# Kernel optimization log

Measured on AMD Instinct MI355X. Metric: run time of the kernel, lower is better.

Reference implementation:

```python
import jax, jax.numpy as jnp
import numpy as np

D, NH, HD = 256, 8, 32          # d_model, heads, head_dim
NPTS, NLAY, FF = 4, 6, 1024     # dec_n_points, decoder layers, ffn dim
BS, HS, WS = 4, 96, 96
N = HS * WS                     # flattened source tokens (single level)
NQ = 300                        # object queries
EPS = 1e-5


def setup_inputs() -> dict:
    key = jax.random.key(0)
    ks = iter(jax.random.split(key, 48))

    def nrm(shape, s=0.05):
        return (jax.random.normal(next(ks), shape) * s).astype(jnp.float32)

    inp = {
        "aps": jax.random.normal(next(ks), (BS, N, D), jnp.float32),
        "dvs": jax.random.normal(next(ks), (BS, N, D), jnp.float32),
        "query_embeds": jax.random.normal(next(ks), (NQ, 2 * D), jnp.float32),
        "valid_ratios": jnp.ones((BS, 2), jnp.float32),
        # fusion gating linears (stored as (in, out); y = x @ W + b)
        "aps_w1": nrm((D, D)), "aps_b1": jnp.zeros((D,), jnp.float32),
        "aps_w2": nrm((D, D)), "aps_b2": jnp.zeros((D,), jnp.float32),
        "dvs_w1": nrm((D, D)), "dvs_b1": jnp.zeros((D,), jnp.float32),
        "dvs_w2": nrm((D, D)), "dvs_b2": jnp.zeros((D,), jnp.float32),
        "ref_w": nrm((D, 2)), "ref_b": jnp.zeros((2,), jnp.float32),
        # per-decoder-layer params, stacked along leading NLAY axis
        "sa_qkv_w": nrm((NLAY, D, 3 * D)), "sa_qkv_b": jnp.zeros((NLAY, 3 * D), jnp.float32),
        "sa_out_w": nrm((NLAY, D, D)), "sa_out_b": jnp.zeros((NLAY, D), jnp.float32),
        "off_w": nrm((NLAY, D, NH * NPTS * 2), 0.01),
        "off_b": nrm((NLAY, NH * NPTS * 2), 2.0),
        "attn_w": nrm((NLAY, D, NH * NPTS)), "attn_b": jnp.zeros((NLAY, NH * NPTS), jnp.float32),
        "val_w": nrm((NLAY, D, D)), "val_b": jnp.zeros((NLAY, D), jnp.float32),
        "cout_w": nrm((NLAY, D, D)), "cout_b": jnp.zeros((NLAY, D), jnp.float32),
        "ln1_w": jnp.ones((NLAY, D), jnp.float32), "ln1_b": jnp.zeros((NLAY, D), jnp.float32),
        "ln2_w": jnp.ones((NLAY, D), jnp.float32), "ln2_b": jnp.zeros((NLAY, D), jnp.float32),
        "ln3_w": jnp.ones((NLAY, D), jnp.float32), "ln3_b": jnp.zeros((NLAY, D), jnp.float32),
        "ffn_w1": nrm((NLAY, D, FF)), "ffn_b1": jnp.zeros((NLAY, FF), jnp.float32),
        "ffn_w2": nrm((NLAY, FF, D)), "ffn_b2": jnp.zeros((NLAY, D), jnp.float32),
        "mask": jnp.zeros((BS, N), bool),
        "spatial_shapes": jnp.array([[HS, WS]], jnp.int32),
    }
    return inp


def _layer_norm(x, w, b):
    mu = jnp.mean(x, -1, keepdims=True)
    var = jnp.mean((x - mu) ** 2, -1, keepdims=True)
    return (x - mu) * jax.lax.rsqrt(var + EPS) * w + b


def _forward(aps, dvs, query_embeds, valid_ratios,
             aps_w1, aps_b1, aps_w2, aps_b2,
             dvs_w1, dvs_b1, dvs_w2, dvs_b2,
             ref_w, ref_b,
             sa_qkv_w, sa_qkv_b, sa_out_w, sa_out_b,
             off_w, off_b, attn_w, attn_b, val_w, val_b, cout_w, cout_b,
             ln1_w, ln1_b, ln2_w, ln2_b, ln3_w, ln3_b,
             ffn_w1, ffn_b1, ffn_w2, ffn_b2,
             mask, spatial_shapes):
    bs = aps.shape[0]
    inv_sqrt_d = np.float32(1.0 / np.sqrt(D))
    # ---- cross-modal gating. Original computes full (N,N) QK^T then sums the
    # last axis; sum_j q_i.k_j == q_i . (sum_j k_j), so we use the O(N*d) form.
    aps_gate = jnp.einsum('bnd,bd->bn', aps @ aps_w1 + aps_b1,
                          jnp.sum(aps @ aps_w2 + aps_b2, axis=1)) * inv_sqrt_d
    dvs_gate = jnp.einsum('bnd,bd->bn', dvs @ dvs_w1 + dvs_b1,
                          jnp.sum(dvs @ dvs_w2 + dvs_b2, axis=1)) * inv_sqrt_d
    gate = jax.nn.softmax(jnp.stack([aps_gate, dvs_gate], -1), -1)  # (bs,N,2)
    src = gate[..., :1] * aps + gate[..., 1:] * dvs

    qpos = jnp.broadcast_to(query_embeds[None, :, :D], (bs, NQ, D))
    out = jnp.broadcast_to(query_embeds[None, :, D:], (bs, NQ, D))
    ref_pts = jax.nn.sigmoid(qpos @ ref_w + ref_b)                 # (bs,NQ,2)

    Hs = spatial_shapes[0, 0]
    Ws = spatial_shapes[0, 1]
    # reference_points[:, :, None] * valid_ratios[:, None][:, None] -> (bs,NQ,1,2)
    rp_in = ref_pts[:, :, None, :] * valid_ratios[:, None, None, :]
    inv_sqrt_hd = np.float32(1.0 / np.sqrt(HD))

    for l in range(NLAY):
        # ---- self attention (q=k=tgt+query_pos, v=tgt)
        qk = out + qpos
        qh = (qk @ sa_qkv_w[l, :, :D] + sa_qkv_b[l, :D]).reshape(bs, NQ, NH, HD)
        kh = (qk @ sa_qkv_w[l, :, D:2 * D] + sa_qkv_b[l, D:2 * D]).reshape(bs, NQ, NH, HD)
        vh = (out @ sa_qkv_w[l, :, 2 * D:] + sa_qkv_b[l, 2 * D:]).reshape(bs, NQ, NH, HD)
        att = jax.nn.softmax(jnp.einsum('bqhd,bkhd->bhqk', qh, kh) * inv_sqrt_hd, -1)
        sa = jnp.einsum('bhqk,bkhd->bqhd', att, vh).reshape(bs, NQ, D) @ sa_out_w[l] + sa_out_b[l]
        out = _layer_norm(out + sa, ln2_w[l], ln2_b[l])

        # ---- MSDeformAttn cross attention (single level)
        q = out + qpos
        value = jnp.where(mask[:, :, None], 0.0, src @ val_w[l] + val_b[l])
        value = value.reshape(bs, -1, NH, HD).transpose(0, 2, 1, 3)   # (bs,NH,N,HD)
        offs = (q @ off_w[l] + off_b[l]).reshape(bs, NQ, NH, 1, NPTS, 2)
        aw = jax.nn.softmax((q @ attn_w[l] + attn_b[l]).reshape(bs, NQ, NH, NPTS), -1)
        normalizer = jnp.stack([Ws, Hs]).astype(q.dtype)              # [W, H]
        loc = (rp_in[:, :, None, :, None, :] + offs / normalizer)[:, :, :, 0]  # (bs,NQ,NH,NPTS,2)
        # bilinear sampling == grid_sample(align_corners=False, padding=zeros)
        x = loc[..., 0] * Ws - 0.5
        y = loc[..., 1] * Hs - 0.5
        x0 = jnp.floor(x); y0 = jnp.floor(y)
        wx1 = x - x0; wy1 = y - y0

        def corner(xi, yi, w):
            valid = (xi >= 0) & (xi <= Ws - 1) & (yi >= 0) & (yi <= Hs - 1)
            idx = (jnp.clip(yi, 0, Hs - 1) * Ws + jnp.clip(xi, 0, Ws - 1)).astype(jnp.int32)
            idx = idx.transpose(0, 2, 1, 3).reshape(bs, NH, NQ * NPTS, 1)
            v = jnp.take_along_axis(value, idx, axis=2)              # (bs,NH,NQ*NPTS,HD)
            v = v.reshape(bs, NH, NQ, NPTS, HD).transpose(0, 2, 1, 3, 4)
            return v * (w * valid)[..., None]

        samp = (corner(x0, y0, (1 - wx1) * (1 - wy1))
                + corner(x0 + 1, y0, wx1 * (1 - wy1))
                + corner(x0, y0 + 1, (1 - wx1) * wy1)
                + corner(x0 + 1, y0 + 1, wx1 * wy1))                 # (bs,NQ,NH,NPTS,HD)
        ca = jnp.einsum('bqhp,bqhpd->bqhd', aw, samp).reshape(bs, NQ, D) @ cout_w[l] + cout_b[l]
        out = _layer_norm(out + ca, ln1_w[l], ln1_b[l])

        # ---- FFN
        ff = jax.nn.relu(out @ ffn_w1[l] + ffn_b1[l]) @ ffn_w2[l] + ffn_b2[l]
        out = _layer_norm(out + ff, ln3_w[l], ln3_b[l])

    # return_intermediate_dec=False -> decoder returns (output, reference_points)
    return out, ref_pts, ref_pts


def reference(aps, dvs, query_embeds, valid_ratios,
              aps_w1, aps_b1, aps_w2, aps_b2,
              dvs_w1, dvs_b1, dvs_w2, dvs_b2,
              ref_w, ref_b,
              sa_qkv_w, sa_qkv_b, sa_out_w, sa_out_b,
              off_w, off_b, attn_w, attn_b, val_w, val_b, cout_w, cout_b,
              ln1_w, ln1_b, ln2_w, ln2_b, ln3_w, ln3_b,
              ffn_w1, ffn_b1, ffn_w2, ffn_b2,
              mask, spatial_shapes):
    return _forward(aps, dvs, query_embeds, valid_ratios,
                    aps_w1, aps_b1, aps_w2, aps_b2,
                    dvs_w1, dvs_b1, dvs_w2, dvs_b2,
                    ref_w, ref_b,
                    sa_qkv_w, sa_qkv_b, sa_out_w, sa_out_b,
                    off_w, off_b, attn_w, attn_b, val_w, val_b, cout_w, cout_b,
                    ln1_w, ln1_b, ln2_w, ln2_b, ln3_w, ln3_b,
                    ffn_w1, ffn_b1, ffn_w2, ffn_b2,
                    mask, spatial_shapes)
```

## Files before the change

kernel.cpp:

```cpp
#include <hip/hip_runtime.h>
#include <math.h>

#define D 256
#define NHD 8
#define HDIM 32
#define NPTS 4
#define NLAY 6
#define FFD 1024
#define BSZ 4
#define NSRC 9216
#define NQ 300
#define NROWS (BSZ*NQ)
#define NVROWS (BSZ*NSRC)
#define CCHK 256
#define VSTRIDE 1536
#define LNEPS 1e-5f

typedef __attribute__((ext_vector_type(8))) short short8v;
typedef __attribute__((ext_vector_type(4))) float f32x4;

#define GLOAD_LDS(g, l) __builtin_amdgcn_global_load_lds( \
    (const __attribute__((address_space(1))) void*)(g), \
    (__attribute__((address_space(3))) void*)(l), 16, 0, 0)

__device__ __forceinline__ unsigned short f2bf(float f){
  unsigned u = __float_as_uint(f);
  unsigned r = (u + 0x7FFFu + ((u>>16)&1u)) >> 16;
  return (unsigned short)r;
}
__device__ __forceinline__ float bf2f(unsigned short u){
  return __uint_as_float(((unsigned)u)<<16);
}

__device__ __forceinline__ float wred_sum(float v){
#pragma unroll
  for(int o=32;o>=1;o>>=1) v += __shfl_xor(v,o,64);
  return v;
}
__device__ __forceinline__ float bred_sum(float v, float* s){
  v = wred_sum(v);
  int lane = threadIdx.x & 63, wid = threadIdx.x >> 6;
  if(lane==0) s[wid]=v;
  __syncthreads();
  float r = s[0]+s[1]+s[2]+s[3];
  __syncthreads();
  return r;
}

__global__ void colsum_partial(const float* __restrict__ aps, const float* __restrict__ dvs,
                               float* __restrict__ pA, float* __restrict__ pD){
  __shared__ float4 sA[4][64]; __shared__ float4 sD[4][64];
  int blk = blockIdx.x; int b = blk / CCHK; int c = blk % CCHK;
  int t = threadIdx.x; int cl = t & 63; int rg = t >> 6;
  const int rows = NSRC / CCHK;
  size_t base = ((size_t)b*NSRC + (size_t)c*rows)*D + cl*4;
  float4 sa = make_float4(0.f,0.f,0.f,0.f), sd = sa;
  for(int r=rg; r<rows; r+=4){
    float4 va = *(const float4*)(aps + base + (size_t)r*D);
    float4 vd = *(const float4*)(dvs + base + (size_t)r*D);
    sa.x+=va.x; sa.y+=va.y; sa.z+=va.z; sa.w+=va.w;
    sd.x+=vd.x; sd.y+=vd.y; sd.z+=vd.z; sd.w+=vd.w;
  }
  sA[rg][cl]=sa; sD[rg][cl]=sd;
  __syncthreads();
  if(t < 64){
    float4 r0=sA[0][t],r1=sA[1][t],r2=sA[2][t],r3=sA[3][t];
    float4 o; o.x=r0.x+r1.x+r2.x+r3.x; o.y=r0.y+r1.y+r2.y+r3.y;
    o.z=r0.z+r1.z+r2.z+r3.z; o.w=r0.w+r1.w+r2.w+r3.w;
    *(float4*)(pA + ((size_t)b*CCHK+c)*D + t*4) = o;
  } else if(t < 128){
    int u=t-64;
    float4 r0=sD[0][u],r1=sD[1][u],r2=sD[2][u],r3=sD[3][u];
    float4 o; o.x=r0.x+r1.x+r2.x+r3.x; o.y=r0.y+r1.y+r2.y+r3.y;
    o.z=r0.z+r1.z+r2.z+r3.z; o.w=r0.w+r1.w+r2.w+r3.w;
    *(float4*)(pD + ((size_t)b*CCHK+c)*D + u*4) = o;
  }
}

__global__ void gate_s2(const float* __restrict__ pA, const float* __restrict__ pD,
                        const float* __restrict__ w2a, const float* __restrict__ b2a,
                        const float* __restrict__ w2d, const float* __restrict__ b2d,
                        const float* __restrict__ b1a, const float* __restrict__ b1d,
                        float* __restrict__ s2, float* __restrict__ cAB){
  __shared__ float sums[D]; __shared__ float red[4];
  int blk = blockIdx.x; int b = blk>>1; int mod = blk&1;
  int t = threadIdx.x;
  const float* pX = mod? pD : pA;
  const float* w2 = mod? w2d : w2a;
  const float* b2 = mod? b2d : b2a;
  const float* b1 = mod? b1d : b1a;
  float s=0.f;
  for(int c=0;c<CCHK;++c) s += pX[((size_t)b*CCHK+c)*D+t];
  sums[t]=s; __syncthreads();
  float v=0.f;
  for(int i=0;i<D;++i) v += sums[i]*w2[(size_t)i*D+t];
  v += (float)NSRC * b2[t];
  s2[(size_t)blk*D + t] = v;
  float c = bred_sum(b1[t]*v, red);
  if(t==0) cAB[mod*BSZ + b] = c;
}

__global__ void gate_t(const float* __restrict__ w1a, const float* __restrict__ w1d,
                       const float* __restrict__ s2,
                       float* __restrict__ tA, float* __restrict__ tD){
  int gw = blockIdx.x*4 + (threadIdx.x>>6);
  int lane = threadIdx.x & 63;
  int i = gw & 255; int bm = gw >> 8;
  int mod = bm & 1, b = bm >> 1;
  const float* w1 = mod? w1d : w1a;
  const float* s2v = s2 + (size_t)bm*D;
  float4 wv = *(const float4*)(w1 + (size_t)i*D + lane*4);
  float4 sv = *(const float4*)(s2v + lane*4);
  float d = wv.x*sv.x + wv.y*sv.y + wv.z*sv.z + wv.w*sv.w;
  d = wred_sum(d);
  if(lane==0){
    if(mod) tD[b*D+i] = d; else tA[b*D+i] = d;
  }
}

__global__ void gate_src(const float* __restrict__ aps, const float* __restrict__ dvs,
                         const float* __restrict__ tA, const float* __restrict__ tD,
                         const float* __restrict__ cAB, unsigned short* __restrict__ srcb){
  int w = threadIdx.x >> 6, lane = threadIdx.x & 63;
  size_t row = (size_t)blockIdx.x*4 + w;
  int b = (int)(row / NSRC);
  const float4* ap = (const float4*)(aps + row*D);
  const float4* dp = (const float4*)(dvs + row*D);
  const float4* tap = (const float4*)(tA + (size_t)b*D);
  const float4* tdp = (const float4*)(tD + (size_t)b*D);
  float4 a = ap[lane], dd = dp[lane], ta = tap[lane], td = tdp[lane];
  float ga = a.x*ta.x + a.y*ta.y + a.z*ta.z + a.w*ta.w;
  float gd = dd.x*td.x + dd.y*td.y + dd.z*td.z + dd.w*td.w;
  ga = (wred_sum(ga) + cAB[b]) * 0.0625f;
  gd = (wred_sum(gd) + cAB[BSZ+b]) * 0.0625f;
  float m = fmaxf(ga,gd);
  float ea = expf(ga-m), ed = expf(gd-m);
  float inv = 1.f/(ea+ed);
  float wa = ea*inv, wd = ed*inv;
  ushort4 o;
  o.x = f2bf(wa*a.x + wd*dd.x); o.y = f2bf(wa*a.y + wd*dd.y);
  o.z = f2bf(wa*a.z + wd*dd.z); o.w = f2bf(wa*a.w + wd*dd.w);
  ((ushort4*)(srcb + row*D))[lane] = o;
}

__global__ void wconv_all(const float* __restrict__ valw, const float* __restrict__ saqkvw,
                          const float* __restrict__ saoutw, const float* __restrict__ coutw,
                          const float* __restrict__ ffw1, const float* __restrict__ ffw2,
                          unsigned short* __restrict__ valT, unsigned short* __restrict__ qkvT,
                          unsigned short* __restrict__ saoutT, unsigned short* __restrict__ coutT,
                          unsigned short* __restrict__ ff1T, unsigned short* __restrict__ ff2T){
  __shared__ float tile[32][33];
  int bid = blockIdx.x;
  const float* W; unsigned short* Bt; int K, N, rel;
  if(bid < 384)      { W=valw;   Bt=valT;   K=256;  N=256;  rel=bid; }
  else if(bid < 1536){ W=saqkvw; Bt=qkvT;   K=256;  N=768;  rel=bid-384; }
  else if(bid < 1920){ W=saoutw; Bt=saoutT; K=256;  N=256;  rel=bid-1536; }
  else if(bid < 2304){ W=coutw;  Bt=coutT;  K=256;  N=256;  rel=bid-1920; }
  else if(bid < 3840){ W=ffw1;   Bt=ff1T;   K=256;  N=1024; rel=bid-2304; }
  else               { W=ffw2;   Bt=ff2T;   K=1024; N=256;  rel=bid-3840; }
  int nk = K>>5, nn = N>>5, tpl = nk*nn;
  int l = rel/tpl, rem = rel%tpl;
  int tk = rem % nk, tn = rem / nk;
  int tx = threadIdx.x & 31, ty = threadIdx.x >> 5;
  const float* Wl = W + (size_t)l*K*N;
  unsigned short* Btl = Bt + (size_t)l*N*K;
#pragma unroll
  for(int i=0;i<4;++i)
    tile[ty+i*8][tx] = Wl[(size_t)(tk*32+ty+i*8)*N + tn*32+tx];
  __syncthreads();
#pragma unroll
  for(int i=0;i<4;++i)
    Btl[(size_t)(tn*32+ty+i*8)*K + tk*32+tx] = f2bf(tile[tx][ty+i*8]);
}

__global__ void init_out_ref(const float* __restrict__ qe, const float* __restrict__ refw,
                             const float* __restrict__ refb,
                             float* __restrict__ outb, unsigned short* __restrict__ out_bf,
                             unsigned short* __restrict__ outpos_bf,
                             float* __restrict__ refp, float* __restrict__ dout){
  __shared__ float red[4];
  int q = blockIdx.x, t = threadIdx.x;
  float pos = qe[(size_t)q*2*D + t];
  float tgt = qe[(size_t)q*2*D + D + t];
  unsigned short tb = f2bf(tgt), tpb = f2bf(tgt+pos);
  for(int b=0;b<BSZ;++b){
    outb[((size_t)b*NQ+q)*D + t] = tgt;
    out_bf[((size_t)b*NQ+q)*D + t] = tb;
    outpos_bf[((size_t)b*NQ+q)*D + t] = tpb;
  }
  float d0 = bred_sum(pos*refw[t*2+0], red);
  float d1 = bred_sum(pos*refw[t*2+1], red);
  if(t<2){
    float dot = (t==0? d0 : d1) + refb[t];
    float r = 1.f/(1.f+expf(-dot));
    refp[q*2+t] = r;
    const size_t o1 = (size_t)BSZ*NQ*D;
    const size_t o2 = o1 + (size_t)BSZ*NQ*2;
    for(int b=0;b<BSZ;++b){
      dout[o1 + (b*NQ+q)*2 + t] = r;
      dout[o2 + (b*NQ+q)*2 + t] = r;
    }
  }
}

__global__ __launch_bounds__(256, 4) void gemmb(
    const unsigned short* __restrict__ A,
    const unsigned short* __restrict__ A2,
    int ncut,
    const unsigned short* __restrict__ Bt,
    const float* __restrict__ bias,
    float* __restrict__ Cf, unsigned short* __restrict__ Cb,
    int M, int K, int N, int relu){
  __shared__ unsigned short As[64][40];
  __shared__ unsigned short Bs[64][40];
  int n0 = blockIdx.x*64, m0 = blockIdx.y*64;
  const unsigned short* Asrc = (A2 && n0 >= ncut) ? A2 : A;
  int t = threadIdx.x, wave = t>>6, lane = t&63;
  int wm = (wave>>1)*32, wn = (wave&1)*32;
  int hi = lane>>4, lo = lane&15;
  int sr = t>>2, sc = (t&3)*8;
  f32x4 acc[2][2];
#pragma unroll
  for(int i=0;i<2;++i)
#pragma unroll
    for(int j=0;j<2;++j)
#pragma unroll
      for(int r=0;r<4;++r) acc[i][j][r]=0.f;
  for(int k0=0;k0<K;k0+=32){
    uint4 av = make_uint4(0,0,0,0);
    int arow = m0+sr;
    if(arow < M) av = *(const uint4*)(Asrc + (size_t)arow*K + k0 + sc);
    *(uint4*)&As[sr][sc] = av;
    *(uint4*)&Bs[sr][sc] = *(const uint4*)(Bt + (size_t)(n0+sr)*K + k0 + sc);
    __syncthreads();
    short8v a0 = *(short8v*)&As[wm+lo][hi*8];
    short8v a1 = *(short8v*)&As[wm+16+lo][hi*8];
    short8v b0 = *(short8v*)&Bs[wn+lo][hi*8];
    short8v b1 = *(short8v*)&Bs[wn+16+lo][hi*8];
    acc[0][0] = __builtin_amdgcn_mfma_f32_16x16x32_bf16(a0,b0,acc[0][0],0,0,0);
    acc[0][1] = __builtin_amdgcn_mfma_f32_16x16x32_bf16(a0,b1,acc[0][1],0,0,0);
    acc[1][0] = __builtin_amdgcn_mfma_f32_16x16x32_bf16(a1,b0,acc[1][0],0,0,0);
    acc[1][1] = __builtin_amdgcn_mfma_f32_16x16x32_bf16(a1,b1,acc[1][1],0,0,0);
    __syncthreads();
  }
#pragma unroll
  for(int mf=0;mf<2;++mf){
#pragma unroll
    for(int nf=0;nf<2;++nf){
      int col = n0 + wn + nf*16 + lo;
      float bv = bias[col];
#pragma unroll
      for(int r=0;r<4;++r){
        int row = m0 + wm + mf*16 + hi*4 + r;
        if(row < M){
          float v = acc[mf][nf][r] + bv;
          if(relu) v = fmaxf(v, 0.f);
          if(Cf) Cf[(size_t)row*N+col] = v;
          if(Cb) Cb[(size_t)row*N+col] = f2bf(v);
        }
      }
    }
  }
}

__global__ __launch_bounds__(256, 4) void mfma_value6(
    const unsigned short* __restrict__ Abf,
    const unsigned short* __restrict__ Bt,
    const float* __restrict__ bias,
    const unsigned char* __restrict__ rowmask,
    unsigned short* __restrict__ C){
  __shared__ unsigned short As[128][32];
  __shared__ unsigned short Bs[128][32];
  int id = blockIdx.x;
  int swz = (id & 7)*432 + (id >> 3);
  int m0 = (swz/12)*128, n0 = (swz%12)*128;
  int t = threadIdx.x;
  int wave = t>>6, lane = t&63;
  int wm = (wave>>1)*64, wn = (wave&1)*64;
  f32x4 acc[4][4];
#pragma unroll
  for(int i=0;i<4;++i)
#pragma unroll
    for(int j=0;j<4;++j)
#pragma unroll
      for(int r=0;r<4;++r) acc[i][j][r]=0.f;

  int colx = ((lane&3) ^ ((lane>>3)&3)) * 8;
  const unsigned short* Ag = Abf + (size_t)(m0 + wave*32 + (lane>>2))*256 + colx;
  const unsigned short* Bg = Bt  + (size_t)(n0 + wave*32 + (lane>>2))*256 + colx;
  unsigned short* Al0 = &As[wave*32][0];
  unsigned short* Al1 = &As[wave*32+16][0];
  unsigned short* Bl0 = &Bs[wave*32][0];
  unsigned short* Bl1 = &Bs[wave*32+16][0];

  int hi = lane>>4, lo = lane&15;
  int sx = (hi ^ ((lo>>1)&3)) * 8;

  for(int k0=0;k0<256;k0+=32){
    GLOAD_LDS(Ag + k0,           Al0);
    GLOAD_LDS(Ag + k0 + 16*256,  Al1);
    GLOAD_LDS(Bg + k0,           Bl0);
    GLOAD_LDS(Bg + k0 + 16*256,  Bl1);
    __syncthreads();
    short8v a[4], bb[4];
#pragma unroll
    for(int mf=0;mf<4;++mf) a[mf]  = *(short8v*)&As[wm+mf*16+lo][sx];
#pragma unroll
    for(int nf=0;nf<4;++nf) bb[nf] = *(short8v*)&Bs[wn+nf*16+lo][sx];
#pragma unroll
    for(int mf=0;mf<4;++mf)
#pragma unroll
      for(int nf=0;nf<4;++nf)
        acc[mf][nf] = __builtin_amdgcn_mfma_f32_16x16x32_bf16(a[mf], bb[nf], acc[mf][nf], 0,0,0);
    __syncthreads();
  }
#pragma unroll
  for(int mf=0;mf<4;++mf){
    int rbase = m0 + wm + mf*16 + (lane>>4)*4;
#pragma unroll
    for(int nf=0;nf<4;++nf){
      int col = n0 + wn + nf*16 + (lane&15);
      float bv = bias[col];
#pragma unroll
      for(int r=0;r<4;++r){
        int row = rbase + r;
        float v = acc[mf][nf][r] + bv;
        if(rowmask[row]) v = 0.f;
        C[(size_t)row*VSTRIDE + col] = f2bf(v);
      }
    }
  }
}

__global__ __launch_bounds__(256) void self_attn_mfma(
    const unsigned short* __restrict__ qkvh,
    unsigned short* __restrict__ sa){
  __shared__ unsigned short P[64][328];
  __shared__ unsigned short Vt[32][328];
  int blk = blockIdx.x;
  int qt = blk % 5; int bh = blk / 5; int h = bh % NHD; int b = bh / NHD;
  int t = threadIdx.x, wv = t>>6, lane = t&63;
  int hi = lane>>4, lo = lane&15;
  {
    int c = t & 31, rb = t >> 5;
    for(int r = rb; r < 320; r += 8){
      unsigned short v = 0;
      if(r < 300) v = qkvh[(size_t)(b*300+r)*768 + 512 + h*32 + c];
      Vt[c][r] = v;
    }
  }
  __syncthreads();
  int m0 = qt*64 + wv*16;
  int qr = m0 + lo; if(qr > 299) qr = 299;
  short8v aq = *(const short8v*)(qkvh + (size_t)(b*300+qr)*768 + h*32 + hi*8);
  f32x4 s[19];
#pragma unroll
  for(int nt=0; nt<19; ++nt){
    int kr = nt*16 + lo; if(kr > 299) kr = 299;
    short8v bk = *(const short8v*)(qkvh + (size_t)(b*300+kr)*768 + 256 + h*32 + hi*8);
    f32x4 z; z[0]=0.f; z[1]=0.f; z[2]=0.f; z[3]=0.f;
    s[nt] = __builtin_amdgcn_mfma_f32_16x16x32_bf16(aq, bk, z, 0,0,0);
  }
  const float kSc = 0.25506009837f;
  float inv[4];
#pragma unroll
  for(int ri=0; ri<4; ++ri){
    float m = -1e30f;
#pragma unroll
    for(int nt=0; nt<19; ++nt){
      if(nt*16+lo < 300) m = fmaxf(m, s[nt][ri]);
    }
#pragma unroll
    for(int o=8;o>=1;o>>=1) m = fmaxf(m, __shfl_xor(m,o,64));
    float sum = 0.f;
#pragma unroll
    for(int nt=0; nt<19; ++nt){
      float p = 0.f;
      if(nt*16+lo < 300) p = exp2f((s[nt][ri]-m)*kSc);
      sum += p;
      P[wv*16 + hi*4 + ri][nt*16 + lo] = f2bf(p);
    }
    P[wv*16 + hi*4 + ri][304 + lo] = 0;
#pragma unroll
    for(int o=8;o>=1;o>>=1) sum += __shfl_xor(sum,o,64);
    inv[ri] = 1.f/sum;
  }
  f32x4 o0, o1;
#pragma unroll
  for(int r=0;r<4;++r){ o0[r]=0.f; o1[r]=0.f; }
#pragma unroll
  for(int kt=0; kt<10; ++kt){
    short8v ap = *(short8v*)&P[wv*16 + lo][kt*32 + hi*8];
    short8v b0 = *(short8v*)&Vt[lo][kt*32 + hi*8];
    short8v b1 = *(short8v*)&Vt[16+lo][kt*32 + hi*8];
    o0 = __builtin_amdgcn_mfma_f32_16x16x32_bf16(ap, b0, o0, 0,0,0);
    o1 = __builtin_amdgcn_mfma_f32_16x16x32_bf16(ap, b1, o1, 0,0,0);
  }
#pragma unroll
  for(int ri=0; ri<4; ++ri){
    int r = m0 + hi*4 + ri;
    if(r < 300){
      size_t base = (size_t)(b*300+r)*256 + h*32;
      sa[base + lo]      = f2bf(o0[ri]*inv[ri]);
      sa[base + 16 + lo] = f2bf(o1[ri]*inv[ri]);
    }
  }
}

__global__ void residual_ln(const float* __restrict__ base, const float* __restrict__ delta,
                            const float* __restrict__ lw, const float* __restrict__ lb,
                            float* __restrict__ dstf, unsigned short* __restrict__ dstb,
                            unsigned short* __restrict__ dstp, const float* __restrict__ qe){
  int w = threadIdx.x >> 6, lane = threadIdx.x & 63;
  size_t row = (size_t)blockIdx.x*4 + w;
  float4 bv = ((const float4*)(base + row*D))[lane];
  float4 dv = ((const float4*)(delta + row*D))[lane];
  float4 v; v.x=bv.x+dv.x; v.y=bv.y+dv.y; v.z=bv.z+dv.z; v.w=bv.w+dv.w;
  float s = wred_sum(v.x+v.y+v.z+v.w);
  float mean = s * (1.f/D);
  float4 c; c.x=v.x-mean; c.y=v.y-mean; c.z=v.z-mean; c.w=v.w-mean;
  float vs = wred_sum(c.x*c.x + c.y*c.y + c.z*c.z + c.w*c.w);
  float inv = rsqrtf(vs*(1.f/D) + LNEPS);
  float4 wv = ((const float4*)lw)[lane];
  float4 lbv = ((const float4*)lb)[lane];
  float4 y; y.x=c.x*inv*wv.x+lbv.x; y.y=c.y*inv*wv.y+lbv.y;
  y.z=c.z*inv*wv.z+lbv.z; y.w=c.w*inv*wv.w+lbv.w;
  ((float4*)(dstf + row*D))[lane] = y;
  if(dstb){
    ushort4 o; o.x=f2bf(y.x); o.y=f2bf(y.y); o.z=f2bf(y.z); o.w=f2bf(y.w);
    ((ushort4*)(dstb + row*D))[lane] = o;
  }
  if(dstp){
    int q = (int)(row % NQ);
    float4 qv = ((const float4*)(qe + (size_t)q*2*D))[lane];
    ushort4 o; o.x=f2bf(y.x+qv.x); o.y=f2bf(y.y+qv.y);
    o.z=f2bf(y.z+qv.z); o.w=f2bf(y.w+qv.w);
    ((ushort4*)(dstp + row*D))[lane] = o;
  }
}

__global__ void deform_attn_ln(const float* __restrict__ base, const float* __restrict__ delta,
                               const float* __restrict__ lnw, const float* __restrict__ lnb,
                               float* __restrict__ outb,
                               const float* __restrict__ qe,
                               const float* __restrict__ offw, const float* __restrict__ offb,
                               const float* __restrict__ attnw, const float* __restrict__ attnb,
                               const unsigned short* __restrict__ value, const float* __restrict__ refp,
                               const float* __restrict__ vr, const int* __restrict__ sshape,
                               unsigned short* __restrict__ ca){
  __shared__ float qrow[D];
  __shared__ float part[96][2];
  __shared__ float proj[96];
  __shared__ float red[4];
  int row = blockIdx.x; int b = row / NQ; int q = row % NQ;
  int t = threadIdx.x;
  float v = base[(size_t)row*D+t] + delta[(size_t)row*D+t];
  float mean = bred_sum(v, red) * (1.f/D);
  float c = v - mean;
  float var = bred_sum(c*c, red) * (1.f/D);
  float y = c * rsqrtf(var + LNEPS) * lnw[t] + lnb[t];
  outb[(size_t)row*D+t] = y;
  qrow[t] = y + qe[(size_t)q*2*D + t];
  __syncthreads();
  if(t < 192){
    int col = t >> 1, half = t & 1;
    float acc = 0.f;
    if(col < 64){
      const float* W = offw;
      for(int k=half*128; k<half*128+128; ++k) acc += qrow[k]*W[(size_t)k*64 + col];
    } else {
      const float* W = attnw; int cc = col-64;
      for(int k=half*128; k<half*128+128; ++k) acc += qrow[k]*W[(size_t)k*32 + cc];
    }
    part[col][half] = acc;
  }
  __syncthreads();
  if(t < 96) proj[t] = part[t][0] + part[t][1] + (t<64 ? offb[t] : attnb[t-64]);
  __syncthreads();

  int h = t>>5, hd = t&31;
  float Hf = (float)sshape[0], Wf = (float)sshape[1];
  int Ws = sshape[1];
  float rx = refp[q*2+0] * vr[b*2+0];
  float ry = refp[q*2+1] * vr[b*2+1];
  const float* lg = &proj[64 + h*4];
  float m = fmaxf(fmaxf(lg[0],lg[1]),fmaxf(lg[2],lg[3]));
  float e[4]; float esum=0.f;
#pragma unroll
  for(int p=0;p<4;++p){ e[p]=expf(lg[p]-m); esum+=e[p]; }
  float einv = 1.f/esum;
  const float* ofr = &proj[h*8];
  const unsigned short* vbase = value + ((size_t)b*NSRC)*VSTRIDE + h*HDIM + hd;
  float acc = 0.f;
#pragma unroll
  for(int p=0;p<NPTS;++p){
    float lx = rx + ofr[p*2+0]/Wf;
    float ly = ry + ofr[p*2+1]/Hf;
    float x = lx*Wf - 0.5f, y2 = ly*Hf - 0.5f;
    float x0 = floorf(x), y0 = floorf(y2);
    float wx = x-x0, wy = y2-y0;
    float sample = 0.f;
#pragma unroll
    for(int cy=0;cy<2;++cy){
#pragma unroll
      for(int cx=0;cx<2;++cx){
        float xi = x0+cx, yi = y0+cy;
        float wgt = (cx? wx : 1.f-wx) * (cy? wy : 1.f-wy);
        bool valid = (xi>=0.f)&&(xi<=Wf-1.f)&&(yi>=0.f)&&(yi<=Hf-1.f);
        if(valid){
          int idx = (int)fminf(fmaxf(yi,0.f),Hf-1.f)*Ws + (int)fminf(fmaxf(xi,0.f),Wf-1.f);
          sample += wgt * bf2f(vbase[(size_t)idx*VSTRIDE]);
        }
      }
    }
    acc += (e[p]*einv) * sample;
  }
  ca[(size_t)row*D + h*HDIM + hd] = f2bf(acc);
}

extern "C" void kernel_launch(void* const* d_in, const int* in_sizes, int n_in,
                              void* d_out, int out_size, void* d_ws, size_t ws_size,
                              hipStream_t stream){
  const float* aps=(const float*)d_in[0];
  const float* dvs=(const float*)d_in[1];
  const float* qe =(const float*)d_in[2];
  const float* vr =(const float*)d_in[3];
  const float* aps_w1=(const float*)d_in[4]; const float* aps_b1=(const float*)d_in[5];
  const float* aps_w2=(const float*)d_in[6]; const float* aps_b2=(const float*)d_in[7];
  const float* dvs_w1=(const float*)d_in[8]; const float* dvs_b1=(const float*)d_in[9];
  const float* dvs_w2=(const float*)d_in[10]; const float* dvs_b2=(const float*)d_in[11];
  const float* ref_w=(const float*)d_in[12]; const float* ref_b=(const float*)d_in[13];
  const float* saqkvw=(const float*)d_in[14]; const float* saqkvb=(const float*)d_in[15];
  const float* saoutw=(const float*)d_in[16]; const float* saoutb=(const float*)d_in[17];
  const float* offw=(const float*)d_in[18]; const float* offb=(const float*)d_in[19];
  const float* attnw=(const float*)d_in[20]; const float* attnb=(const float*)d_in[21];
  const float* valw=(const float*)d_in[22]; const float* valb=(const float*)d_in[23];
  const float* coutw=(const float*)d_in[24]; const float* coutb=(const float*)d_in[25];
  const float* ln1w=(const float*)d_in[26]; const float* ln1b=(const float*)d_in[27];
  const float* ln2w=(const float*)d_in[28]; const float* ln2b=(const float*)d_in[29];
  const float* ln3w=(const float*)d_in[30]; const float* ln3b=(const float*)d_in[31];
  const float* ffw1=(const float*)d_in[32]; const float* ffb1=(const float*)d_in[33];
  const float* ffw2=(const float*)d_in[34]; const float* ffb2=(const float*)d_in[35];
  const unsigned char* mask=(const unsigned char*)d_in[36];
  const int* sshape=(const int*)d_in[37];
  float* out = (float*)d_out;

  char* wsb = (char*)d_ws;
  size_t o = 0;
  unsigned short* srcb   = (unsigned short*)(wsb+o); o += (size_t)NVROWS*D*2;
  unsigned short* valT   = (unsigned short*)(wsb+o); o += (size_t)NLAY*D*D*2;
  unsigned short* qkvT   = (unsigned short*)(wsb+o); o += (size_t)NLAY*3*D*D*2;
  unsigned short* saoutT = (unsigned short*)(wsb+o); o += (size_t)NLAY*D*D*2;
  unsigned short* coutT  = (unsigned short*)(wsb+o); o += (size_t)NLAY*D*D*2;
  unsigned short* ff1T   = (unsigned short*)(wsb+o); o += (size_t)NLAY*D*FFD*2;
  unsigned short* ff2T   = (unsigned short*)(wsb+o); o += (size_t)NLAY*FFD*D*2;
  unsigned short* value  = (unsigned short*)(wsb+o); o += (size_t)NVROWS*VSTRIDE*2;
  float* pA    = (float*)(wsb+o); o += (size_t)BSZ*CCHK*D*4;
  float* pD    = (float*)(wsb+o); o += (size_t)BSZ*CCHK*D*4;
  float* s2    = (float*)(wsb+o); o += 2*BSZ*D*4;
  float* tA    = (float*)(wsb+o); o += BSZ*D*4;
  float* tD    = (float*)(wsb+o); o += BSZ*D*4;
  float* cAB   = (float*)(wsb+o); o += 16*4;
  float* refp  = (float*)(wsb+o); o += NQ*2*4;
  float* outb  = (float*)(wsb+o); o += (size_t)NROWS*D*4;
  float* tmpb  = (float*)(wsb+o); o += (size_t)NROWS*D*4;
  unsigned short* out_bf    = (unsigned short*)(wsb+o); o += (size_t)NROWS*D*2;
  unsigned short* outpos_bf = (unsigned short*)(wsb+o); o += (size_t)NROWS*D*2;
  unsigned short* qkvh_bf   = (unsigned short*)(wsb+o); o += (size_t)NROWS*3*D*2;
  unsigned short* sa_bf     = (unsigned short*)(wsb+o); o += (size_t)NROWS*D*2;
  unsigned short* ca_bf     = (unsigned short*)(wsb+o); o += (size_t)NROWS*D*2;
  unsigned short* ffh_bf    = (unsigned short*)(wsb+o); o += (size_t)NROWS*FFD*2;

  colsum_partial<<<BSZ*CCHK,256,0,stream>>>(aps,dvs,pA,pD);
  gate_s2<<<2*BSZ,256,0,stream>>>(pA,pD,aps_w2,aps_b2,dvs_w2,dvs_b2,aps_b1,dvs_b1,s2,cAB);
  gate_t<<<512,256,0,stream>>>(aps_w1,dvs_w1,s2,tA,tD);
  gate_src<<<NVROWS/4,256,0,stream>>>(aps,dvs,tA,tD,cAB,srcb);
  wconv_all<<<5376,256,0,stream>>>(valw,saqkvw,saoutw,coutw,ffw1,ffw2,
                                   valT,qkvT,saoutT,coutT,ff1T,ff2T);
  init_out_ref<<<NQ,256,0,stream>>>(qe,ref_w,ref_b,outb,out_bf,outpos_bf,refp,out);
  mfma_value6<<<(NVROWS/128)*(VSTRIDE/128),256,0,stream>>>(srcb, valT, valb, mask, value);

  dim3 gqkv(12,19), g256(4,19), gffu(16,19);

  for(int l=0;l<NLAY;++l){
    const unsigned short* qkvTl = qkvT + (size_t)l*3*D*D;
    const float* bqkv = saqkvb + (size_t)l*3*D;
    gemmb<<<gqkv,256,0,stream>>>(outpos_bf, out_bf, 512, qkvTl, bqkv,
                                 nullptr, qkvh_bf, NROWS, D, 3*D, 0);
    self_attn_mfma<<<BSZ*NHD*5,256,0,stream>>>(qkvh_bf, sa_bf);
    gemmb<<<g256,256,0,stream>>>(sa_bf, nullptr, 0, saoutT+(size_t)l*D*D, saoutb+(size_t)l*D,
                                 tmpb, nullptr, NROWS, D, D, 0);

    deform_attn_ln<<<NROWS,256,0,stream>>>(outb, tmpb, ln2w+(size_t)l*D, ln2b+(size_t)l*D,
                                           outb, qe,
                                           offw+(size_t)l*D*64, offb+(size_t)l*64,
                                           attnw+(size_t)l*D*32, attnb+(size_t)l*32,
                                           value + (size_t)l*D, refp, vr, sshape, ca_bf);
    gemmb<<<g256,256,0,stream>>>(ca_bf, nullptr, 0, coutT+(size_t)l*D*D, coutb+(size_t)l*D,
                                 tmpb, nullptr, NROWS, D, D, 0);
    residual_ln<<<NROWS/4,256,0,stream>>>(outb,tmpb,ln1w+(size_t)l*D,ln1b+(size_t)l*D,
                                          outb,out_bf,nullptr,qe);

    gemmb<<<gffu,256,0,stream>>>(out_bf, nullptr, 0, ff1T+(size_t)l*D*FFD, ffb1+(size_t)l*FFD,
                                 nullptr, ffh_bf, NROWS, D, FFD, 1);
    gemmb<<<g256,256,0,stream>>>(ffh_bf, nullptr, 0, ff2T+(size_t)l*FFD*D, ffb2+(size_t)l*D,
                                 tmpb, nullptr, NROWS, FFD, D, 0);
    if(l==NLAY-1)
      residual_ln<<<NROWS/4,256,0,stream>>>(outb,tmpb,ln3w+(size_t)l*D,ln3b+(size_t)l*D,
                                            out,nullptr,nullptr,qe);
    else
      residual_ln<<<NROWS/4,256,0,stream>>>(outb,tmpb,ln3w+(size_t)l*D,ln3b+(size_t)l*D,
                                            outb,out_bf,outpos_bf,qe);
  }
}
```

Before: 724.0 us.

## Stage 256-wide K chunks in gemmb via direct-to-LDS loads with XOR swizzle

```diff
diff --git a/kernel.cpp b/kernel.cpp
--- a/kernel.cpp
+++ b/kernel.cpp
@@ -203,7 +203,7 @@
   }
 }
 
-__global__ __launch_bounds__(256, 4) void gemmb(
+__global__ __launch_bounds__(256) void gemmb(
     const unsigned short* __restrict__ A,
     const unsigned short* __restrict__ A2,
     int ncut,
@@ -211,14 +211,14 @@
     const float* __restrict__ bias,
     float* __restrict__ Cf, unsigned short* __restrict__ Cb,
     int M, int K, int N, int relu){
-  __shared__ unsigned short As[64][40];
-  __shared__ unsigned short Bs[64][40];
+  __shared__ unsigned short As[64][256];
+  __shared__ unsigned short Bs[64][256];
   int n0 = blockIdx.x*64, m0 = blockIdx.y*64;
   const unsigned short* Asrc = (A2 && n0 >= ncut) ? A2 : A;
   int t = threadIdx.x, wave = t>>6, lane = t&63;
   int wm = (wave>>1)*32, wn = (wave&1)*32;
   int hi = lane>>4, lo = lane&15;
-  int sr = t>>2, sc = (t&3)*8;
+  int lrow2 = lane>>5, lslot = lane&31;
   f32x4 acc[2][2];
 #pragma unroll
   for(int i=0;i<2;++i)
@@ -226,23 +226,33 @@
     for(int j=0;j<2;++j)
 #pragma unroll
       for(int r=0;r<4;++r) acc[i][j][r]=0.f;
-  for(int k0=0;k0<K;k0+=32){
-    uint4 av = make_uint4(0,0,0,0);
-    int arow = m0+sr;
-    if(arow < M) av = *(const uint4*)(Asrc + (size_t)arow*K + k0 + sc);
-    *(uint4*)&As[sr][sc] = av;
-    *(uint4*)&Bs[sr][sc] = *(const uint4*)(Bt + (size_t)(n0+sr)*K + k0 + sc);
+
+  int sx8 = ((lo&7))*8;
+  for(int k0=0;k0<K;k0+=256){
+#pragma unroll
+    for(int i=0;i<8;++i){
+      int rt = wave*16 + 2*i + lrow2;
+      int col = ((lslot ^ (rt&7)))*8;
+      int ga = m0+rt; if(ga >= M) ga = M-1;
+      GLOAD_LDS(Asrc + (size_t)ga*K + k0 + col, &As[wave*16 + 2*i][0]);
+      GLOAD_LDS(Bt + (size_t)(n0+rt)*K + k0 + col, &Bs[wave*16 + 2*i][0]);
+    }
     __syncthreads();
-    short8v a0 = *(short8v*)&As[wm+lo][hi*8];
-    short8v a1 = *(short8v*)&As[wm+16+lo][hi*8];
-    short8v b0 = *(short8v*)&Bs[wn+lo][hi*8];
-    short8v b1 = *(short8v*)&Bs[wn+16+lo][hi*8];
-    acc[0][0] = __builtin_amdgcn_mfma_f32_16x16x32_bf16(a0,b0,acc[0][0],0,0,0);
-    acc[0][1] = __builtin_amdgcn_mfma_f32_16x16x32_bf16(a0,b1,acc[0][1],0,0,0);
-    acc[1][0] = __builtin_amdgcn_mfma_f32_16x16x32_bf16(a1,b0,acc[1][0],0,0,0);
-    acc[1][1] = __builtin_amdgcn_mfma_f32_16x16x32_bf16(a1,b1,acc[1][1],0,0,0);
-    __syncthreads();
-  }
+#pragma unroll
+    for(int kk=0;kk<8;++kk){
+      int ps = (((kk*4+hi) ^ (lo&7)))*8;
+      short8v a0 = *(short8v*)&As[wm+lo][ps];
+      short8v a1 = *(short8v*)&As[wm+16+lo][ps];
+      short8v b0 = *(short8v*)&Bs[wn+lo][ps];
+      short8v b1 = *(short8v*)&Bs[wn+16+lo][ps];
+      acc[0][0] = __builtin_amdgcn_mfma_f32_16x16x32_bf16(a0,b0,acc[0][0],0,0,0);
+      acc[0][1] = __builtin_amdgcn_mfma_f32_16x16x32_bf16(a0,b1,acc[0][1],0,0,0);
+      acc[1][0] = __builtin_amdgcn_mfma_f32_16x16x32_bf16(a1,b0,acc[1][0],0,0,0);
+      acc[1][1] = __builtin_amdgcn_mfma_f32_16x16x32_bf16(a1,b1,acc[1][1],0,0,0);
+    }
+    if(k0 + 256 < K) __syncthreads();
+  }
+  (void)sx8;
 #pragma unroll
   for(int mf=0;mf<2;++mf){
 #pragma unroll
@@ -263,7 +273,7 @@
   }
 }
 
-__global__ __launch_bounds__(256, 4) void mfma_value6(
+__global__ __launch_bounds__(256) void mfma_value6(
     const unsigned short* __restrict__ Abf,
     const unsigned short* __restrict__ Bt,
     const float* __restrict__ bias,
```

Result: faster. 617.8 us (-14.7%).
